# Optimization experiments

Hardware: AMD Instinct MI355X
Metric: run time of the kernel (lower is better)

Reference implementation:

```python
import jax, jax.numpy as jnp
import numpy as np

N_NODES = 50000
N_EDGES = 600000
IN_DIM, HID_DIM, OUT_DIM = 128, 256, 40


def setup_inputs() -> dict:
    key = jax.random.key(0)
    ks = jax.random.split(key, 10)
    x = jax.random.normal(ks[0], (N_NODES, IN_DIM), dtype=jnp.float32)
    edge_index = jax.random.randint(ks[1], (2, N_EDGES), 0, N_NODES, dtype=jnp.int64)
    def lin(k, out_d, in_d):
        s = 1.0 / np.sqrt(in_d)
        return jax.random.uniform(k, (out_d, in_d), jnp.float32, -s, s)
    # SAGEConv: lin_l (on aggregated neighbors, with bias) + lin_r (on self, no bias)
    params = {
        "Wl1": lin(ks[2], HID_DIM, IN_DIM), "bl1": jnp.zeros((HID_DIM,), jnp.float32), "Wr1": lin(ks[3], HID_DIM, IN_DIM),
        "Wl2": lin(ks[4], HID_DIM, HID_DIM), "bl2": jnp.zeros((HID_DIM,), jnp.float32), "Wr2": lin(ks[5], HID_DIM, HID_DIM),
        "Wl3": lin(ks[6], OUT_DIM, HID_DIM), "bl3": jnp.zeros((OUT_DIM,), jnp.float32), "Wr3": lin(ks[7], OUT_DIM, HID_DIM),
    }
    return {"x": x, "edge_index": edge_index, **params}


def _sage_conv(x, src, dst, Wl, bl, Wr):
    # mean-aggregate source features into destination nodes
    n = x.shape[0]
    agg = jax.ops.segment_sum(x[src], dst, num_segments=n)          # [N, d_in]
    cnt = jax.ops.segment_sum(jnp.ones_like(dst, dtype=x.dtype), dst, num_segments=n)
    mean = agg / jnp.maximum(cnt, 1.0)[:, None]
    return mean @ Wl.T + bl + x @ Wr.T


def reference(x, edge_index, Wl1, bl1, Wr1, Wl2, bl2, Wr2, Wl3, bl3, Wr3):
    src, dst = edge_index[0], edge_index[1]
    h = _sage_conv(x, src, dst, Wl1, bl1, Wr1)
    h = jax.nn.relu(h)  # dropout is identity in eval mode
    h = _sage_conv(h, src, dst, Wl2, bl2, Wr2)
    h = jax.nn.relu(h)
    h = _sage_conv(h, src, dst, Wl3, bl3, Wr3)
    return jax.nn.log_softmax(h, axis=1)
```

## Files before the change

### kernel.cpp

```cpp
#include <hip/hip_runtime.h>
#include <hip/hip_bf16.h>

#define IN_DIM 128
#define HID_DIM 256
#define OUT_DIM 40
#define SCAN_CHUNK 2048

typedef __attribute__((ext_vector_type(8))) __bf16 bf16x8;
typedef __attribute__((ext_vector_type(4))) float f32x4;

__device__ inline ushort f2bf(float f) {
    uint u = __builtin_bit_cast(uint, f);
    u = (u + 0x7fff + ((u >> 16) & 1)) >> 16;
    return (ushort)u;
}
__device__ inline float bfl(uint u) { return __builtin_bit_cast(float, u << 16); }
__device__ inline float bfh(uint u) { return __builtin_bit_cast(float, u & 0xffff0000u); }

__device__ inline void gload_lds16(const ushort* g, ushort* l) {
    __builtin_amdgcn_global_load_lds((const __attribute__((address_space(1))) void*)g,
                                     (__attribute__((address_space(3))) void*)l, 16, 0, 0);
}

__device__ inline int xcd_swizzle(int b, int G) {
    int q = G >> 3, r = G & 7;
    int xcd = b & 7, j = b >> 3;
    return (xcd < r ? xcd * (q + 1) : r * (q + 1) + (xcd - r) * q) + j;
}

__global__ __launch_bounds__(256) void prep_kernel(
    const float* __restrict__ x, ushort* __restrict__ xb, int n4, int XB,
    const float* __restrict__ Wl1, const float* __restrict__ Wr1,
    const float* __restrict__ Wl2, const float* __restrict__ Wr2,
    const float* __restrict__ Wl3, const float* __restrict__ Wr3,
    ushort* __restrict__ o1l, ushort* __restrict__ o1r,
    ushort* __restrict__ o2l, ushort* __restrict__ o2r,
    ushort* __restrict__ o3l, ushort* __restrict__ o3r, int WB,
    const int* __restrict__ dst, int* __restrict__ cnt, int E) {
    int b = blockIdx.x;
    if (b < XB) {
        int i = b * 256 + threadIdx.x;
        if (i < n4) {
            float4 v = ((const float4*)x)[i];
            uint2 o;
            o.x = (uint)f2bf(v.x) | ((uint)f2bf(v.y) << 16);
            o.y = (uint)f2bf(v.z) | ((uint)f2bf(v.w) << 16);
            ((uint2*)xb)[i] = o;
        }
        return;
    }
    b -= XB;
    if (b < WB) {
        int idx = b * 256 + threadIdx.x;
        if (idx < 32768) {
            int j = idx & 7, ln = (idx >> 3) & 15, quad = (idx >> 7) & 3;
            int kk = (idx >> 9) & 3, ct = (idx >> 11) & 3, cb = idx >> 13;
            int o = cb * 64 + ct * 16 + ln;
            int k = kk * 32 + quad * 8 + j;
            o1l[idx] = f2bf(Wl1[o * 128 + k]);
            o1r[idx] = f2bf(Wr1[o * 128 + k]);
            return;
        }
        idx -= 32768;
        if (idx < 65536) {
            int j = idx & 7, ln = (idx >> 3) & 15, quad = (idx >> 7) & 3;
            int kk = (idx >> 9) & 7, ct = (idx >> 12) & 3, cb = idx >> 14;
            int o = cb * 64 + ct * 16 + ln;
            int k = kk * 32 + quad * 8 + j;
            o2l[idx] = f2bf(Wl2[o * 256 + k]);
            o2r[idx] = f2bf(Wr2[o * 256 + k]);
            return;
        }
        idx -= 65536;
        if (idx < 48 * 256) {
            int row = idx >> 8;
            int col = idx & 255;
            ushort vl = 0, vr = 0;
            if (row < OUT_DIM) {
                vl = f2bf(Wl3[row * 256 + col]);
                vr = f2bf(Wr3[row * 256 + col]);
            }
            o3l[idx] = vl;
            o3r[idx] = vr;
        }
        return;
    }
    b -= WB;
    int e = b * 256 + threadIdx.x;
    if (e < E) atomicAdd(&cnt[dst[e]], 1);
}

__global__ __launch_bounds__(256) void scan_pass1(const int* __restrict__ cnt,
                                                  int* __restrict__ bsum, int N) {
    __shared__ int red[256];
    const int base = blockIdx.x * SCAN_CHUNK;
    int s = 0;
    for (int i = threadIdx.x; i < SCAN_CHUNK; i += 256) {
        int idx = base + i;
        if (idx < N) s += cnt[idx];
    }
    red[threadIdx.x] = s;
    __syncthreads();
    for (int o = 128; o > 0; o >>= 1) {
        if (threadIdx.x < o) red[threadIdx.x] += red[threadIdx.x + o];
        __syncthreads();
    }
    if (threadIdx.x == 0) bsum[blockIdx.x] = red[0];
}

__global__ __launch_bounds__(256) void scan_pass3(const int* __restrict__ cnt,
                                                  const int* __restrict__ bsum,
                                                  int* __restrict__ rowptr,
                                                  int* __restrict__ cursor,
                                                  float* __restrict__ inv,
                                                  int N, int E, int SB) {
    __shared__ int ls[256];
    __shared__ int boff;
    if (threadIdx.x == 0) {
        int r = 0;
        for (int i = 0; i < blockIdx.x; ++i) r += bsum[i];
        boff = r;
    }
    const int tbase = blockIdx.x * SCAN_CHUNK + threadIdx.x * 8;
    int c[8];
    int s = 0;
#pragma unroll
    for (int j = 0; j < 8; ++j) {
        int idx = tbase + j;
        c[j] = (idx < N) ? cnt[idx] : 0;
        s += c[j];
    }
    ls[threadIdx.x] = s;
    __syncthreads();
    for (int o = 1; o < 256; o <<= 1) {
        int u = (threadIdx.x >= o) ? ls[threadIdx.x - o] : 0;
        __syncthreads();
        ls[threadIdx.x] += u;
        __syncthreads();
    }
    int run = boff + ls[threadIdx.x] - s;
#pragma unroll
    for (int j = 0; j < 8; ++j) {
        int idx = tbase + j;
        if (idx < N) {
            rowptr[idx] = run;
            cursor[idx] = run;
            inv[idx] = 1.0f / fmaxf((float)c[j], 1.0f);
            run += c[j];
        }
    }
    if (blockIdx.x == 0 && threadIdx.x == 0) rowptr[N] = E;
}

__global__ __launch_bounds__(256) void fill_kernel(const int* __restrict__ src,
                                                   const int* __restrict__ dst,
                                                   int* __restrict__ cursor,
                                                   int* __restrict__ srcs, int E) {
    int e = blockIdx.x * 256 + threadIdx.x;
    if (e < E) {
        int pos = atomicAdd(&cursor[dst[e]], 1);
        srcs[pos] = src[e];
    }
}

template <int D>
__global__ __launch_bounds__(256) void gather_mean_bf(const ushort* __restrict__ feat,
                                                      const int* __restrict__ rowptr,
                                                      const int* __restrict__ srcs,
                                                      const float* __restrict__ inv,
                                                      ushort* __restrict__ out, int N) {
    constexpr int LPN = D / 8;
    constexpr int NPW = 64 / LPN;
    constexpr int NPB = 4 * NPW;
    const int wave = threadIdx.x >> 6;
    const int lane = threadIdx.x & 63;
    const int sub = lane / LPN;
    const int sl = lane % LPN;
    const int n = blockIdx.x * NPB + wave * NPW + sub;
    const bool alive = n < N;
    const int beg = alive ? rowptr[n] : 0;
    const int end = alive ? rowptr[n + 1] : 0;
    const int col = sl * 8;

    float a0 = 0.f, a1 = 0.f, a2 = 0.f, a3 = 0.f;
    float a4 = 0.f, a5 = 0.f, a6 = 0.f, a7 = 0.f;
    int e = beg;
    for (; e + 3 < end; e += 4) {
        uint4 q[4];
#pragma unroll
        for (int j = 0; j < 4; ++j)
            q[j] = *(const uint4*)&feat[(long long)srcs[e + j] * D + col];
#pragma unroll
        for (int j = 0; j < 4; ++j) {
            a0 += bfl(q[j].x); a1 += bfh(q[j].x);
            a2 += bfl(q[j].y); a3 += bfh(q[j].y);
            a4 += bfl(q[j].z); a5 += bfh(q[j].z);
            a6 += bfl(q[j].w); a7 += bfh(q[j].w);
        }
    }
    for (; e < end; ++e) {
        uint4 q = *(const uint4*)&feat[(long long)srcs[e] * D + col];
        a0 += bfl(q.x); a1 += bfh(q.x);
        a2 += bfl(q.y); a3 += bfh(q.y);
        a4 += bfl(q.z); a5 += bfh(q.z);
        a6 += bfl(q.w); a7 += bfh(q.w);
    }
    if (alive) {
        const float sc = inv[n];
        uint4 o;
        o.x = (uint)f2bf(a0 * sc) | ((uint)f2bf(a1 * sc) << 16);
        o.y = (uint)f2bf(a2 * sc) | ((uint)f2bf(a3 * sc) << 16);
        o.z = (uint)f2bf(a4 * sc) | ((uint)f2bf(a5 * sc) << 16);
        o.w = (uint)f2bf(a6 * sc) | ((uint)f2bf(a7 * sc) << 16);
        *(uint4*)&out[(long long)n * D + col] = o;
    }
}

template <int K, bool RELU, bool OUTBF>
__global__ __launch_bounds__(512, 4) void sage_gemm_mfma(const ushort* __restrict__ Amean,
                                                         const ushort* __restrict__ Aself,
                                                         const ushort* __restrict__ Wl,
                                                         const float* __restrict__ bias,
                                                         const ushort* __restrict__ Wr,
                                                         void* __restrict__ outv, int N, int O,
                                                         int G) {
    constexpr int NK = K / 32;
    constexpr int TILE = 64 * K;
    constexpr int CHUNKS = TILE / 512;
    __shared__ __align__(16) ushort Ws[2 * TILE];

    const int tid = threadIdx.x;
    const int wave = tid >> 6;
    const int lane = tid & 63;
    const int ln = lane & 15;
    const int quad = lane >> 4;

    const int wid = xcd_swizzle(blockIdx.x, G);
    const int cb = wid & 3;
    const int bm0 = (wid >> 2) * 256;

    {
        const ushort* gl = Wl + (size_t)cb * TILE;
        const ushort* gr = Wr + (size_t)cb * TILE;
#pragma unroll
        for (int c = wave; c < CHUNKS; c += 8) {
            gload_lds16(gl + c * 512 + lane * 8, &Ws[c * 512]);
            gload_lds16(gr + c * 512 + lane * 8, &Ws[TILE + c * 512]);
        }
    }

    int arow[2];
#pragma unroll
    for (int rt = 0; rt < 2; ++rt) {
        int r = bm0 + wave * 32 + rt * 16 + ln;
        arow[rt] = min(r, N - 1);
    }

    bf16x8 areg[NK][2];
#pragma unroll
    for (int kk = 0; kk < NK; ++kk)
#pragma unroll
        for (int rt = 0; rt < 2; ++rt)
            areg[kk][rt] = *(const bf16x8*)&Amean[(long long)arow[rt] * K + kk * 32 + quad * 8];

    f32x4 acc[2][4] = {};
    __syncthreads();

#pragma unroll
    for (int kk = 0; kk < NK; ++kk) {
#pragma unroll
        for (int ct = 0; ct < 4; ++ct) {
            bf16x8 b = *(const bf16x8*)&Ws[((ct * NK + kk) * 64 + lane) * 8];
#pragma unroll
            for (int rt = 0; rt < 2; ++rt)
                acc[rt][ct] = __builtin_amdgcn_mfma_f32_16x16x32_bf16(areg[kk][rt], b, acc[rt][ct], 0, 0, 0);
        }
#pragma unroll
        for (int rt = 0; rt < 2; ++rt)
            areg[kk][rt] = *(const bf16x8*)&Aself[(long long)arow[rt] * K + kk * 32 + quad * 8];
    }

#pragma unroll
    for (int kk = 0; kk < NK; ++kk) {
#pragma unroll
        for (int ct = 0; ct < 4; ++ct) {
            bf16x8 b = *(const bf16x8*)&Ws[TILE + ((ct * NK + kk) * 64 + lane) * 8];
#pragma unroll
            for (int rt = 0; rt < 2; ++rt)
                acc[rt][ct] = __builtin_amdgcn_mfma_f32_16x16x32_bf16(areg[kk][rt], b, acc[rt][ct], 0, 0, 0);
        }
    }

#pragma unroll
    for (int rt = 0; rt < 2; ++rt) {
        int rbase = bm0 + wave * 32 + rt * 16 + quad * 4;
#pragma unroll
        for (int ct = 0; ct < 4; ++ct) {
            int col = cb * 64 + ct * 16 + ln;
            if (col >= O) continue;
            float bv = bias[col];
#pragma unroll
            for (int r = 0; r < 4; ++r) {
                int row = rbase + r;
                if (row >= N) continue;
                float v = acc[rt][ct][r] + bv;
                if (RELU) v = fmaxf(v, 0.f);
                if (OUTBF)
                    ((ushort*)outv)[(long long)row * O + col] = f2bf(v);
                else
                    ((float*)outv)[(long long)row * O + col] = v;
            }
        }
    }
}

template <int K>
__global__ __launch_bounds__(256, 3) void sage_gemm_pre(const ushort* __restrict__ A0,
                                                        const ushort* __restrict__ Wl,
                                                        const ushort* __restrict__ Wr,
                                                        ushort* __restrict__ P,
                                                        float* __restrict__ S, int N, int O) {
    constexpr int KP = 2 * K + 8;
    constexpr int NK = K / 32;
    __shared__ __align__(16) ushort Ws[48 * KP];

    const int tid = threadIdx.x;
    const int wave = tid >> 6;
    const int lane = tid & 63;
    const int ln = lane & 15;
    const int quad = lane >> 4;
    const int bm0 = blockIdx.x * 64;

    const int arow = min(bm0 + wave * 16 + ln, N - 1);

#pragma unroll
    for (int i = tid; i < 48 * (K / 8); i += 256) {
        int row = i / (K / 8);
        int c8 = (i % (K / 8)) * 8;
        *(ulonglong2*)&Ws[row * KP + c8] =
            *(const ulonglong2*)&Wl[(long long)row * K + c8];
        *(ulonglong2*)&Ws[row * KP + K + c8] =
            *(const ulonglong2*)&Wr[(long long)row * K + c8];
    }
    __syncthreads();

#pragma unroll
    for (int phase = 0; phase < 2; ++phase) {
        f32x4 acc[3] = {};
#pragma unroll
        for (int kk = 0; kk < NK; ++kk) {
            bf16x8 a = *(const bf16x8*)&A0[(long long)arow * K + kk * 32 + quad * 8];
#pragma unroll
            for (int ct = 0; ct < 3; ++ct) {
                bf16x8 b = *(const bf16x8*)&Ws[(ct * 16 + ln) * KP + phase * K + kk * 32 + quad * 8];
                acc[ct] = __builtin_amdgcn_mfma_f32_16x16x32_bf16(a, b, acc[ct], 0, 0, 0);
            }
        }
        int rbase = bm0 + wave * 16 + quad * 4;
#pragma unroll
        for (int ct = 0; ct < 3; ++ct) {
            int col = ct * 16 + ln;
            if (col >= O) continue;
#pragma unroll
            for (int r = 0; r < 4; ++r) {
                int row = rbase + r;
                if (row >= N) continue;
                if (phase == 0)
                    P[(long long)row * O + col] = f2bf(acc[ct][r]);
                else
                    S[(long long)row * O + col] = acc[ct][r];
            }
        }
    }
}

__global__ __launch_bounds__(256) void agg_bias_lsm(const ushort* __restrict__ P,
                                                    const float* __restrict__ S,
                                                    const float* __restrict__ bias,
                                                    const int* __restrict__ rowptr,
                                                    const int* __restrict__ srcs,
                                                    const float* __restrict__ inv,
                                                    float* __restrict__ out, int N) {
    const int wave = threadIdx.x >> 6;
    const int lane = threadIdx.x & 63;
    const int n = blockIdx.x * 4 + wave;
    if (n >= N) return;
    const int beg = rowptr[n];
    const int end = rowptr[n + 1];
    const bool act = lane < OUT_DIM;
    const int cidx = act ? lane : 0;

    float acc = 0.f;
    int e = beg;
    for (; e + 3 < end; e += 4) {
        int s0 = srcs[e], s1 = srcs[e + 1], s2 = srcs[e + 2], s3 = srcs[e + 3];
        float v0 = __builtin_bit_cast(float, (uint)P[(long long)s0 * OUT_DIM + cidx] << 16);
        float v1 = __builtin_bit_cast(float, (uint)P[(long long)s1 * OUT_DIM + cidx] << 16);
        float v2 = __builtin_bit_cast(float, (uint)P[(long long)s2 * OUT_DIM + cidx] << 16);
        float v3 = __builtin_bit_cast(float, (uint)P[(long long)s3 * OUT_DIM + cidx] << 16);
        acc += (v0 + v1) + (v2 + v3);
    }
    for (; e < end; ++e)
        acc += __builtin_bit_cast(float, (uint)P[(long long)srcs[e] * OUT_DIM + cidx] << 16);

    float v = act ? (acc * inv[n] + S[(long long)n * OUT_DIM + lane] + bias[lane]) : -INFINITY;
    float m = v;
#pragma unroll
    for (int o = 32; o > 0; o >>= 1) m = fmaxf(m, __shfl_xor(m, o, 64));
    float ex = act ? expf(v - m) : 0.f;
    float sm = ex;
#pragma unroll
    for (int o = 32; o > 0; o >>= 1) sm += __shfl_xor(sm, o, 64);
    float ls = logf(sm);
    if (act) out[(long long)n * OUT_DIM + lane] = v - m - ls;
}

extern "C" void kernel_launch(void* const* d_in, const int* in_sizes, int n_in,
                              void* d_out, int out_size, void* d_ws, size_t ws_size,
                              hipStream_t stream) {
    const float* x   = (const float*)d_in[0];
    const int*   ei  = (const int*)d_in[1];
    const float* Wl1 = (const float*)d_in[2];
    const float* bl1 = (const float*)d_in[3];
    const float* Wr1 = (const float*)d_in[4];
    const float* Wl2 = (const float*)d_in[5];
    const float* bl2 = (const float*)d_in[6];
    const float* Wr2 = (const float*)d_in[7];
    const float* Wl3 = (const float*)d_in[8];
    const float* bl3 = (const float*)d_in[9];
    const float* Wr3 = (const float*)d_in[10];
    float* out = (float*)d_out;

    const int N = in_sizes[0] / IN_DIM;
    const int E = in_sizes[1] / 2;
    const int* src = ei;
    const int* dst = ei + E;

    char* w = (char*)d_ws;
    size_t off = 0;
    auto alloc = [&](size_t bytes) {
        void* p = w + off;
        off = (off + bytes + 255) & ~(size_t)255;
        return p;
    };
    ushort* xb   = (ushort*)alloc((size_t)N * IN_DIM * 2);
    ushort* M    = (ushort*)alloc((size_t)N * HID_DIM * 2);
    ushort* H1   = (ushort*)alloc((size_t)N * HID_DIM * 2);
    ushort* H2   = (ushort*)alloc((size_t)N * HID_DIM * 2);
    ushort* P3   = (ushort*)alloc((size_t)N * OUT_DIM * 2);
    float*  S3   = (float*)alloc((size_t)N * OUT_DIM * 4);
    float*  inv  = (float*)alloc((size_t)N * 4);
    int*    cnt  = (int*)alloc((size_t)N * 4);
    int*    rowptr = (int*)alloc((size_t)(N + 1) * 4);
    int*    cursor = (int*)alloc((size_t)N * 4);
    int*    srcs = (int*)alloc((size_t)E * 4);
    int*    bsum = (int*)alloc(256 * 4);
    ushort* Wl1b = (ushort*)alloc(256 * 128 * 2);
    ushort* Wr1b = (ushort*)alloc(256 * 128 * 2);
    ushort* Wl2b = (ushort*)alloc(256 * 256 * 2);
    ushort* Wr2b = (ushort*)alloc(256 * 256 * 2);
    ushort* Wl3b = (ushort*)alloc(48 * 256 * 2);
    ushort* Wr3b = (ushort*)alloc(48 * 256 * 2);

    const int n4 = N * IN_DIM / 4;
    const int XB = (n4 + 255) / 256;
    const int WB = (32768 + 65536 + 48 * 256 + 255) / 256;
    const int HB = (E + 255) / 256;
    hipMemsetAsync(cnt, 0, (size_t)N * sizeof(int), stream);
    prep_kernel<<<XB + WB + HB, 256, 0, stream>>>(
        x, xb, n4, XB,
        Wl1, Wr1, Wl2, Wr2, Wl3, Wr3,
        Wl1b, Wr1b, Wl2b, Wr2b, Wl3b, Wr3b, WB,
        dst, cnt, E);

    const int SB = (N + SCAN_CHUNK - 1) / SCAN_CHUNK;
    scan_pass1<<<SB, 256, 0, stream>>>(cnt, bsum, N);
    scan_pass3<<<SB, 256, 0, stream>>>(cnt, bsum, rowptr, cursor, inv, N, E, SB);
    fill_kernel<<<HB, 256, 0, stream>>>(src, dst, cursor, srcs, E);

    const int gm = (N + 255) / 256;
    const int G = 4 * gm;
    const int gg128 = (N + 15) / 16;
    const int gg256 = (N + 7) / 8;
    const int gg = (N + 3) / 4;

    gather_mean_bf<IN_DIM><<<gg128, 256, 0, stream>>>(xb, rowptr, srcs, inv, M, N);
    sage_gemm_mfma<IN_DIM, true, true><<<G, 512, 0, stream>>>(
        M, xb, Wl1b, bl1, Wr1b, H1, N, HID_DIM, G);

    gather_mean_bf<HID_DIM><<<gg256, 256, 0, stream>>>(H1, rowptr, srcs, inv, M, N);
    sage_gemm_mfma<HID_DIM, true, true><<<G, 512, 0, stream>>>(
        M, H1, Wl2b, bl2, Wr2b, H2, N, HID_DIM, G);

    sage_gemm_pre<HID_DIM><<<(N + 63) / 64, 256, 0, stream>>>(
        H2, Wl3b, Wr3b, P3, S3, N, OUT_DIM);
    agg_bias_lsm<<<gg, 256, 0, stream>>>(P3, S3, bl3, rowptr, srcs, inv, out, N);
}
```

Measured before the change: 344.3 us.

## Widen GEMM column tile to 128 and stage Wl/Wr sequentially in LDS

The SAGE GEMM kernel now computes 128 output columns per block instead of 64, which halves the grid and the number of times each A row is re-read from global memory. Wl and Wr tiles are loaded one after another into the same LDS buffer, with a barrier in between, so the LDS footprint per block stays bounded. The accumulators double to 2x8 per wave, and the launch bound drops to 2 blocks per CU to make room for the extra registers. The costs are lower occupancy and an extra barrier. The prefetch of Aself that used to overlap the Wl MFMAs is gone, so that load is now serialized.

```diff
diff --git a/kernel.cpp b/kernel.cpp
--- a/kernel.cpp
+++ b/kernel.cpp
@@ -217,7 +217,7 @@
 }
 
 template <int K, bool RELU, bool OUTBF>
-__global__ __launch_bounds__(512, 4) void sage_gemm_mfma(const ushort* __restrict__ Amean,
+__global__ __launch_bounds__(512, 2) void sage_gemm_mfma(const ushort* __restrict__ Amean,
                                                          const ushort* __restrict__ Aself,
                                                          const ushort* __restrict__ Wl,
                                                          const float* __restrict__ bias,
@@ -225,9 +225,9 @@
                                                          void* __restrict__ outv, int N, int O,
                                                          int G) {
     constexpr int NK = K / 32;
-    constexpr int TILE = 64 * K;
-    constexpr int CHUNKS = TILE / 512;
-    __shared__ __align__(16) ushort Ws[2 * TILE];
+    constexpr int TILE2 = 128 * K;
+    constexpr int CHUNKS = TILE2 / 512;
+    __shared__ __align__(16) ushort Ws[TILE2];
 
     const int tid = threadIdx.x;
     const int wave = tid >> 6;
@@ -236,18 +236,8 @@
     const int quad = lane >> 4;
 
     const int wid = xcd_swizzle(blockIdx.x, G);
-    const int cb = wid & 3;
-    const int bm0 = (wid >> 2) * 256;
-
-    {
-        const ushort* gl = Wl + (size_t)cb * TILE;
-        const ushort* gr = Wr + (size_t)cb * TILE;
-#pragma unroll
-        for (int c = wave; c < CHUNKS; c += 8) {
-            gload_lds16(gl + c * 512 + lane * 8, &Ws[c * 512]);
-            gload_lds16(gr + c * 512 + lane * 8, &Ws[TILE + c * 512]);
-        }
-    }
+    const int c2 = wid & 1;
+    const int bm0 = (wid >> 1) * 256;
 
     int arow[2];
 #pragma unroll
@@ -256,38 +246,36 @@
         arow[rt] = min(r, N - 1);
     }
 
-    bf16x8 areg[NK][2];
-#pragma unroll
-    for (int kk = 0; kk < NK; ++kk)
-#pragma unroll
-        for (int rt = 0; rt < 2; ++rt)
-            areg[kk][rt] = *(const bf16x8*)&Amean[(long long)arow[rt] * K + kk * 32 + quad * 8];
-
-    f32x4 acc[2][4] = {};
-    __syncthreads();
-
-#pragma unroll
-    for (int kk = 0; kk < NK; ++kk) {
-#pragma unroll
-        for (int ct = 0; ct < 4; ++ct) {
-            bf16x8 b = *(const bf16x8*)&Ws[((ct * NK + kk) * 64 + lane) * 8];
+    f32x4 acc[2][8] = {};
+
+#pragma unroll
+    for (int p = 0; p < 2; ++p) {
+        const ushort* __restrict__ A = p ? Aself : Amean;
+        const ushort* __restrict__ gsrc = (p ? Wr : Wl) + (size_t)c2 * TILE2;
+
+        if (p) __syncthreads();
+#pragma unroll
+        for (int c = wave; c < CHUNKS; c += 8)
+            gload_lds16(gsrc + c * 512 + lane * 8, &Ws[c * 512]);
+
+        bf16x8 areg[NK][2];
+#pragma unroll
+        for (int kk = 0; kk < NK; ++kk)
 #pragma unroll
             for (int rt = 0; rt < 2; ++rt)
-                acc[rt][ct] = __builtin_amdgcn_mfma_f32_16x16x32_bf16(areg[kk][rt], b, acc[rt][ct], 0, 0, 0);
-        }
-#pragma unroll
-        for (int rt = 0; rt < 2; ++rt)
-            areg[kk][rt] = *(const bf16x8*)&Aself[(long long)arow[rt] * K + kk * 32 + quad * 8];
-    }
-
-#pragma unroll
-    for (int kk = 0; kk < NK; ++kk) {
-#pragma unroll
-        for (int ct = 0; ct < 4; ++ct) {
-            bf16x8 b = *(const bf16x8*)&Ws[TILE + ((ct * NK + kk) * 64 + lane) * 8];
-#pragma unroll
-            for (int rt = 0; rt < 2; ++rt)
-                acc[rt][ct] = __builtin_amdgcn_mfma_f32_16x16x32_bf16(areg[kk][rt], b, acc[rt][ct], 0, 0, 0);
+                areg[kk][rt] = *(const bf16x8*)&A[(long long)arow[rt] * K + kk * 32 + quad * 8];
+
+        __syncthreads();
+
+#pragma unroll
+        for (int kk = 0; kk < NK; ++kk) {
+#pragma unroll
+            for (int ct = 0; ct < 8; ++ct) {
+                bf16x8 b = *(const bf16x8*)&Ws[((ct * NK + kk) * 64 + lane) * 8];
+#pragma unroll
+                for (int rt = 0; rt < 2; ++rt)
+                    acc[rt][ct] = __builtin_amdgcn_mfma_f32_16x16x32_bf16(areg[kk][rt], b, acc[rt][ct], 0, 0, 0);
+            }
         }
     }
 
@@ -295,8 +283,8 @@
     for (int rt = 0; rt < 2; ++rt) {
         int rbase = bm0 + wave * 32 + rt * 16 + quad * 4;
 #pragma unroll
-        for (int ct = 0; ct < 4; ++ct) {
-            int col = cb * 64 + ct * 16 + ln;
+        for (int ct = 0; ct < 8; ++ct) {
+            int col = c2 * 128 + ct * 16 + ln;
             if (col >= O) continue;
             float bv = bias[col];
 #pragma unroll
@@ -479,7 +467,7 @@
     fill_kernel<<<HB, 256, 0, stream>>>(src, dst, cursor, srcs, E);
 
     const int gm = (N + 255) / 256;
-    const int G = 4 * gm;
+    const int G = 2 * gm;
     const int gg128 = (N + 15) / 16;
     const int gg256 = (N + 7) / 8;
     const int gg = (N + 3) / 4;
```

Result: no change. 341.9 us (-0.7%).
